# Kernel optimization log

Hardware: AMD Instinct MI355X
Metric: run time of the kernel (lower is better)

The kernel has to match this reference:

```python
import jax, jax.numpy as jnp
import numpy as np

N_HEAD = 12
N_EMBD = 768
HEAD_DIM = N_EMBD // N_HEAD
B, S = 4, 2048


def setup_inputs() -> dict:
    key = jax.random.key(0)
    k1, k2, k3, k4, k5 = jax.random.split(key, 5)
    x = jax.random.normal(k1, (B, S, N_EMBD), dtype=jnp.float32)
    # causal additive mask: 1.0 where attention is disallowed (strictly upper triangle)
    mask = (1.0 - jnp.tril(jnp.ones((S, S), dtype=jnp.float32)))[None, None, :, :]
    scale = 0.02
    W_attn = jax.random.normal(k2, (N_EMBD, 3 * N_EMBD), dtype=jnp.float32) * scale
    b_attn = jnp.zeros((3 * N_EMBD,), dtype=jnp.float32)
    W_proj = jax.random.normal(k3, (N_EMBD, N_EMBD), dtype=jnp.float32) * scale
    b_proj = jnp.zeros((N_EMBD,), dtype=jnp.float32)
    return {"x": x, "mask": mask, "W_attn": W_attn, "b_attn": b_attn,
            "W_proj": W_proj, "b_proj": b_proj}


def reference(x, mask, W_attn, b_attn, W_proj, b_proj):
    Bn, Sn, _ = x.shape
    qkv = x @ W_attn + b_attn                      # [B,S,3E]
    q, k, v = jnp.split(qkv, 3, axis=-1)           # each [B,S,E]

    def heads(t):
        return t.reshape(Bn, Sn, N_HEAD, HEAD_DIM).transpose(0, 2, 1, 3)  # [B,H,S,D]

    q, k, v = heads(q), heads(k), heads(v)
    attn = jnp.einsum('bhqd,bhkd->bhqk', q, k) / jnp.sqrt(jnp.float32(HEAD_DIM))
    attn = attn + mask * (-1e9)
    attn = jax.nn.softmax(attn, axis=-1)
    # dropout in inference mode = identity
    out = jnp.einsum('bhqk,bhkd->bhqd', attn, v)   # [B,H,S,D]
    out = out.transpose(0, 2, 1, 3).reshape(Bn, Sn, N_EMBD)
    return out @ W_proj + b_proj
```

## Files before the change

### kernel.cpp

```cpp
#include <hip/hip_runtime.h>
#include <stdint.h>

#define NHEAD 12
#define HDIM  64
#define EMB   768
#define N3    2304
#define SEQ   2048
#define BATCH 4
#define MROWS 8192

#define QSCALE 0.18033688011112042f

typedef __bf16 bf16_t;
typedef __bf16 bf16x8 __attribute__((ext_vector_type(8)));
typedef __bf16 bf16x4 __attribute__((ext_vector_type(4)));
typedef short  s16x4  __attribute__((ext_vector_type(4)));
typedef float  f32x4  __attribute__((ext_vector_type(4)));

__device__ __forceinline__ void gld_lds16(void* lds, const void* g) {
    __builtin_amdgcn_global_load_lds((const __attribute__((address_space(1))) void*)g,
                                     (__attribute__((address_space(3))) void*)lds,
                                     16, 0, 0);
}

__device__ __forceinline__ float fast_exp2(float x) {
    return __builtin_amdgcn_exp2f(x);
}

__device__ __forceinline__ f32x4 mfma16_bf16(bf16x4 a, bf16x4 b, f32x4 c) {
#if __has_builtin(__builtin_amdgcn_mfma_f32_16x16x16_bf16)
    return __builtin_amdgcn_mfma_f32_16x16x16_bf16(a, b, c, 0, 0, 0);
#else
    union U { bf16x4 h; s16x4 s; };
    U ua, ub; ua.h = a; ub.h = b;
    return __builtin_amdgcn_mfma_f32_16x16x16bf16_1k(ua.s, ub.s, c, 0, 0, 0);
#endif
}

__global__ __launch_bounds__(256) void cvt_x_k(const float* __restrict__ x,
                                               bf16_t* __restrict__ xb, int n8) {
    int idx    = blockIdx.x * blockDim.x + threadIdx.x;
    int stride = gridDim.x * blockDim.x;
    for (int i = idx; i < n8; i += stride) {
        float4 a = ((const float4*)x)[i * 2];
        float4 b = ((const float4*)x)[i * 2 + 1];
        bf16x8 v;
        v[0] = (bf16_t)a.x; v[1] = (bf16_t)a.y; v[2] = (bf16_t)a.z; v[3] = (bf16_t)a.w;
        v[4] = (bf16_t)b.x; v[5] = (bf16_t)b.y; v[6] = (bf16_t)b.z; v[7] = (bf16_t)b.w;
        ((bf16x8*)xb)[i] = v;
    }
}

__global__ __launch_bounds__(256) void transpose_cvt_k(
    const float* __restrict__ W, bf16_t* __restrict__ WT, int K, int N) {
    __shared__ float tile[32][33];
    const int n0 = blockIdx.x * 32, k0 = blockIdx.y * 32;
    const int tx = threadIdx.x & 31, ty = threadIdx.x >> 5;
#pragma unroll
    for (int i = 0; i < 32; i += 8)
        tile[ty + i][tx] = W[(size_t)(k0 + ty + i) * N + (n0 + tx)];
    __syncthreads();
#pragma unroll
    for (int i = 0; i < 32; i += 8)
        WT[(size_t)(n0 + ty + i) * K + (k0 + tx)] = (bf16_t)tile[tx][ty + i];
}

template<int MODE>
__global__ __launch_bounds__(256) void gemm_kernel(
    const bf16_t* __restrict__ Av,
    const bf16_t* __restrict__ BT,
    const float* __restrict__ bias,
    float* __restrict__ out,
    bf16_t* __restrict__ qbuf,
    bf16_t* __restrict__ kbuf,
    bf16_t* __restrict__ vbuf,
    int Ncols)
{
    const int K = 768;
    __shared__ alignas(16) bf16_t As[2][128 * 32];
    __shared__ alignas(16) bf16_t Bs[2][128 * 32];

    const int tid    = threadIdx.x;
    const int wave   = tid >> 6;
    const int lane   = tid & 63;
    const int lane15 = lane & 15;
    const int quad   = lane >> 4;

    const int mBase = blockIdx.y * 128;
    const int nBase = blockIdx.x * 128;
    const int wm = (wave >> 1) * 64;
    const int wn = (wave & 1) * 64;

    f32x4 acc[4][4];
#pragma unroll
    for (int i = 0; i < 4; i++)
#pragma unroll
        for (int j = 0; j < 4; j++) acc[i][j] = (f32x4){0.f, 0.f, 0.f, 0.f};

    const bf16_t* aSrc = Av + (size_t)mBase * K;
    const bf16_t* bSrc = BT + (size_t)nBase * K;

    const int srow = lane >> 2;
    const int sch  = lane & 3;

    auto issueA = [&](int k0, int buf) {
#pragma unroll
        for (int p = 0; p < 2; p++) {
            int r0  = p * 64 + wave * 16;
            int row = r0 + srow;
            int lch = sch ^ (row & 3);
            gld_lds16(&As[buf][r0 * 32], aSrc + (size_t)row * K + k0 + lch * 8);
        }
    };
    auto issueB = [&](int k0, int buf) {
#pragma unroll
        for (int p = 0; p < 2; p++) {
            int r0  = p * 64 + wave * 16;
            int row = r0 + srow;
            int lch = sch ^ (row & 3);
            gld_lds16(&Bs[buf][r0 * 32], bSrc + (size_t)row * K + k0 + lch * 8);
        }
    };

    issueA(0, 0);
    issueB(0, 0);

    for (int k0 = 0, it = 0; k0 < K; k0 += 32, it++) {
        const int buf = it & 1;
        __syncthreads();
        if (k0 + 32 < K) {
            issueB(k0 + 32, buf ^ 1);
            issueA(k0 + 32, buf ^ 1);
        }

        bf16x8 aF[4], bF[4];
#pragma unroll
        for (int t = 0; t < 4; t++) {
            int ra = wm + t * 16 + lane15;
            int rb = wn + t * 16 + lane15;
            aF[t] = *(const bf16x8*)&As[buf][ra * 32 + (quad ^ (ra & 3)) * 8];
            bF[t] = *(const bf16x8*)&Bs[buf][rb * 32 + (quad ^ (rb & 3)) * 8];
        }
#pragma unroll
        for (int i = 0; i < 4; i++)
#pragma unroll
            for (int j = 0; j < 4; j++)
                acc[i][j] = __builtin_amdgcn_mfma_f32_16x16x32_bf16(aF[i], bF[j], acc[i][j], 0, 0, 0);
    }

    const int region = (MODE == 1) ? (nBase / EMB) : 0;
#pragma unroll
    for (int i = 0; i < 4; i++) {
#pragma unroll
        for (int j = 0; j < 4; j++) {
            int gn = nBase + wn + j * 16 + lane15;
            float bv = bias[gn];
            if (MODE == 0) {
#pragma unroll
                for (int r = 0; r < 4; r++) {
                    int gm = mBase + wm + i * 16 + quad * 4 + r;
                    out[(size_t)gm * Ncols + gn] = acc[i][j][r] + bv;
                }
            } else if (region == 2) {
                int within = gn - 2 * EMB;
                int h = within >> 6, d = within & 63;
                int gm0 = mBase + wm + i * 16 + quad * 4;
                int b = gm0 >> 11, s = gm0 & 2047;
                int bh = b * NHEAD + h;
                bf16x4 v4;
#pragma unroll
                for (int r = 0; r < 4; r++) v4[r] = (bf16_t)(acc[i][j][r] + bv);
                *(bf16x4*)&vbuf[((size_t)bh * HDIM + d) * SEQ + s] = v4;
            } else {
                bf16_t* dst = (region == 0) ? qbuf : kbuf;
                const float scale = (region == 0) ? QSCALE : 1.0f;
                int within = gn - region * EMB;
                int h = within >> 6, d = within & 63;
#pragma unroll
                for (int r = 0; r < 4; r++) {
                    int gm = mBase + wm + i * 16 + quad * 4 + r;
                    int b = gm >> 11, s = gm & 2047;
                    int bh = b * NHEAD + h;
                    dst[((size_t)bh * SEQ + s) * HDIM + d] = (bf16_t)((acc[i][j][r] + bv) * scale);
                }
            }
        }
    }
}

__global__ __launch_bounds__(256) void attn_kernel(
    const bf16_t* __restrict__ qbuf,
    const bf16_t* __restrict__ kbuf,
    const bf16_t* __restrict__ vtbuf,
    bf16_t* __restrict__ obuf)
{
    __shared__ alignas(16) bf16_t Ks[2][64 * 64];
    __shared__ alignas(16) bf16_t Vs[2][64 * 64];
    __shared__ alignas(16) bf16_t Plds[4][16 * 72];

    const int tid    = threadIdx.x;
    const int wave   = tid >> 6;
    const int lane   = tid & 63;
    const int lane15 = lane & 15;
    const int quad   = lane >> 4;

    const int bh = blockIdx.x >> 4;
    const int j  = blockIdx.x & 15;

    const bf16_t* Qp = qbuf  + (size_t)bh * SEQ * HDIM;
    const bf16_t* Kp = kbuf  + (size_t)bh * SEQ * HDIM;
    const bf16_t* Vp = vtbuf + (size_t)bh * HDIM * SEQ;
    bf16_t* pl = &Plds[wave][0];
    const int b = bh / NHEAD, h = bh % NHEAD;

    const int srow8 = lane >> 3;
    const int sch8  = lane & 7;

    auto issueKV = [&](int kb, int buf) {
#pragma unroll
        for (int p = 0; p < 2; p++) {
            int r0  = p * 32 + wave * 8;
            int row = r0 + srow8;
            int lch = sch8 ^ (row & 7);
            gld_lds16(&Ks[buf][r0 * 64], Kp + (size_t)(kb + row) * HDIM + lch * 8);
            gld_lds16(&Vs[buf][r0 * 64], Vp + (size_t)row * SEQ + kb + lch * 8);
        }
    };

    for (int seg = 0; seg < 2; seg++) {
        const int qt = seg ? (31 - j) : j;
        const int q0 = qt * 64 + wave * 16;

        const bf16x8 qf0 = *(const bf16x8*)&Qp[(size_t)(q0 + lane15) * HDIM + quad * 8];
        const bf16x8 qf1 = *(const bf16x8*)&Qp[(size_t)(q0 + lane15) * HDIM + 32 + quad * 8];

        float lrow = 0.f;
        f32x4 oT[4];
#pragma unroll
        for (int t = 0; t < 4; t++) oT[t] = (f32x4){0.f, 0.f, 0.f, 0.f};

        const int nT = qt + 1;
        __syncthreads();
        issueKV(0, 0);

        for (int kt = 0; kt < nT; kt++) {
            const int buf = kt & 1;
            __syncthreads();
            if (kt + 1 < nT) issueKV((kt + 1) * 64, buf ^ 1);

            const int kb = kt * 64;

            f32x4 sT[4];
#pragma unroll
            for (int kg = 0; kg < 4; kg++) {
                sT[kg] = (f32x4){0.f, 0.f, 0.f, 0.f};
                int row = kg * 16 + lane15;
                bf16x8 kf0 = *(const bf16x8*)&Ks[buf][row * 64 + ((quad    ) ^ (row & 7)) * 8];
                bf16x8 kf1 = *(const bf16x8*)&Ks[buf][row * 64 + ((quad + 4) ^ (row & 7)) * 8];
                sT[kg] = __builtin_amdgcn_mfma_f32_16x16x32_bf16(kf0, qf0, sT[kg], 0, 0, 0);
                sT[kg] = __builtin_amdgcn_mfma_f32_16x16x32_bf16(kf1, qf1, sT[kg], 0, 0, 0);
            }

            if (kb + 64 > q0) {
                const int query = q0 + lane15;
#pragma unroll
                for (int kg = 0; kg < 4; kg++) {
                    int key0 = kb + kg * 16 + quad * 4;
#pragma unroll
                    for (int r = 0; r < 4; r++)
                        sT[kg][r] = (key0 + r <= query) ? sT[kg][r] : -1e30f;
                }
            }

            bf16x4 pf[4];
#pragma unroll
            for (int kg = 0; kg < 4; kg++) {
#pragma unroll
                for (int r = 0; r < 4; r++) sT[kg][r] = fast_exp2(sT[kg][r]);
                lrow += (sT[kg][0] + sT[kg][1]) + (sT[kg][2] + sT[kg][3]);
                bf16x4 v;
#pragma unroll
                for (int r = 0; r < 4; r++) v[r] = (bf16_t)sT[kg][r];
                pf[kg] = v;
            }

#pragma unroll
            for (int t = 0; t < 4; t++) {
                int vrow = t * 16 + lane15;
#pragma unroll
                for (int kg = 0; kg < 4; kg++) {
                    int c    = kg * 2 + (quad >> 1);
                    int phys = c ^ (vrow & 7);
                    bf16x4 vf = *(const bf16x4*)&Vs[buf][vrow * 64 + phys * 8 + (quad & 1) * 4];
                    oT[t] = mfma16_bf16(vf, pf[kg], oT[t]);
                }
            }
        }

        lrow += __shfl_xor(lrow, 16, 64);
        lrow += __shfl_xor(lrow, 32, 64);
        const float inv = 1.0f / lrow;

#pragma unroll
        for (int t = 0; t < 4; t++)
#pragma unroll
            for (int r = 0; r < 4; r++)
                pl[lane15 * 72 + t * 16 + quad * 4 + r] = (bf16_t)(oT[t][r] * inv);

        const int qrow = lane >> 2;
        const int ch   = lane & 3;
        bf16_t* orow = &obuf[((size_t)(b * SEQ + q0 + qrow)) * EMB + h * HDIM];
#pragma unroll
        for (int p = 0; p < 2; p++) {
            bf16x8 v = *(const bf16x8*)&pl[qrow * 72 + (ch + p * 4) * 8];
            *(bf16x8*)&orow[(ch + p * 4) * 8] = v;
        }
    }
}

extern "C" void kernel_launch(void* const* d_in, const int* in_sizes, int n_in,
                              void* d_out, int out_size, void* d_ws, size_t ws_size,
                              hipStream_t stream) {
    const float* x      = (const float*)d_in[0];
    const float* W_attn = (const float*)d_in[2];
    const float* b_attn = (const float*)d_in[3];
    const float* W_proj = (const float*)d_in[4];
    const float* b_proj = (const float*)d_in[5];
    float* out = (float*)d_out;

    bf16_t* ws  = (bf16_t*)d_ws;
    bf16_t* WaT = ws;
    bf16_t* WpT = WaT + (size_t)N3 * EMB;
    bf16_t* Qb  = WpT + (size_t)EMB * EMB;
    bf16_t* Kb  = Qb + (size_t)BATCH * NHEAD * SEQ * HDIM;
    bf16_t* Vt  = Kb + (size_t)BATCH * NHEAD * SEQ * HDIM;
    bf16_t* Ob  = Vt + (size_t)BATCH * NHEAD * SEQ * HDIM;
    bf16_t* xb  = Ob;

    transpose_cvt_k<<<dim3(N3 / 32, EMB / 32), 256, 0, stream>>>(W_attn, WaT, EMB, N3);
    transpose_cvt_k<<<dim3(EMB / 32, EMB / 32), 256, 0, stream>>>(W_proj, WpT, EMB, EMB);
    cvt_x_k<<<1536, 256, 0, stream>>>(x, xb, MROWS * EMB / 8);

    gemm_kernel<1><<<dim3(N3 / 128, MROWS / 128), 256, 0, stream>>>(
        xb, WaT, b_attn, nullptr, Qb, Kb, Vt, N3);

    attn_kernel<<<BATCH * NHEAD * 16, 256, 0, stream>>>(Qb, Kb, Vt, Ob);

    gemm_kernel<0><<<dim3(EMB / 128, MROWS / 128), 256, 0, stream>>>(
        Ob, WpT, b_proj, out, nullptr, nullptr, nullptr, EMB);
}
```

Measured before the change: 246.1 us.

## Add dedicated 256x256-tile pipelined QKV GEMM kernel with 8 waves

Replaces the generic 128x128 GEMM used for the QKV projection with a dedicated kernel. It uses 256x256 output tiles, 512 threads, a K-step of 64 with double-buffered direct-to-LDS loads, and phased prefetch interleaved with MFMA work under s_setprio. It also remaps block indices so that consecutive blocks share data in cache. The goal is more data reuse per loaded tile and better overlap of memory loads with compute. In exchange, register and LDS pressure rises (256KB LDS per block is not possible; uses 2*2*128*64*2*2=128KB), and there are only 288 blocks, so occupancy and tail effects may suffer.

```diff
diff --git a/kernel.cpp b/kernel.cpp
--- a/kernel.cpp
+++ b/kernel.cpp
@@ -65,15 +65,176 @@
         WT[(size_t)(n0 + ty + i) * K + (k0 + tx)] = (bf16_t)tile[tx][ty + i];
 }
 
+__global__ __launch_bounds__(512, 2) void qkv_kernel(
+    const bf16_t* __restrict__ Av,
+    const bf16_t* __restrict__ BT,
+    const float*  __restrict__ bias,
+    bf16_t* __restrict__ qbuf,
+    bf16_t* __restrict__ kbuf,
+    bf16_t* __restrict__ vbuf)
+{
+    __shared__ alignas(16) bf16_t As[2][2][128 * 64];
+    __shared__ alignas(16) bf16_t Bs[2][2][128 * 64];
+
+    const int tid    = threadIdx.x;
+    const int wave   = tid >> 6;
+    const int lane   = tid & 63;
+    const int lane15 = lane & 15;
+    const int quad   = lane >> 4;
+    const int wr     = wave >> 2;
+    const int wc     = wave & 3;
+
+    const int bid  = blockIdx.x;
+    const int swz  = (bid & 7) * 36 + (bid >> 3);
+    const int mBase = (swz / 9) * 256;
+    const int nBase = (swz % 9) * 256;
+
+    const int rr = tid >> 3;
+    const int ch = (tid & 7) ^ (rr & 7);
+    const bf16_t* aBase = Av + (size_t)mBase * 768;
+    const bf16_t* bBase = BT + (size_t)nBase * 768;
+
+    auto stageA = [&](int kt, int h) {
+        const int buf = kt & 1;
+#pragma unroll
+        for (int p = 0; p < 2; p++) {
+            const bf16_t* src = aBase + (size_t)(h * 128 + p * 64 + rr) * 768 + kt * 64 + ch * 8;
+            gld_lds16(&As[buf][h][p * 4096 + wave * 512], src);
+        }
+    };
+    auto stageB = [&](int kt, int h) {
+        const int buf = kt & 1;
+#pragma unroll
+        for (int p = 0; p < 2; p++) {
+            const bf16_t* src = bBase + (size_t)(h * 128 + p * 64 + rr) * 768 + kt * 64 + ch * 8;
+            gld_lds16(&Bs[buf][h][p * 4096 + wave * 512], src);
+        }
+    };
+
+    f32x4 acc[8][4];
+#pragma unroll
+    for (int m = 0; m < 8; m++)
+#pragma unroll
+        for (int n = 0; n < 4; n++) acc[m][n] = (f32x4){0.f, 0.f, 0.f, 0.f};
+
+    bf16x8 bF[4][2];
+
+    stageA(0, 0); stageA(0, 1); stageB(0, 0); stageB(0, 1); stageB(1, 0);
+
+    for (int t = 0; t < 12; ++t) {
+        const int buf = t & 1;
+        const bf16_t* Ah = &As[buf][wr][0];
+        const bf16_t* Bh = &Bs[buf][wc >> 1][0];
+
+        if (t < 11) {
+            stageB(t + 1, 1);
+            asm volatile("s_waitcnt vmcnt(4)" ::: "memory");
+        } else {
+            asm volatile("s_waitcnt vmcnt(0)" ::: "memory");
+        }
+        __builtin_amdgcn_sched_barrier(0);
+        __builtin_amdgcn_s_barrier();
+
+#pragma unroll
+        for (int n = 0; n < 4; ++n) {
+            const int rb = (wc & 1) * 64 + n * 16 + lane15;
+#pragma unroll
+            for (int kk = 0; kk < 2; ++kk)
+                bF[n][kk] = *(const bf16x8*)&Bh[rb * 64 + (((kk * 4 + quad) ^ (rb & 7)) * 8)];
+        }
+        {
+            bf16x8 aF[2][2];
+#pragma unroll
+            for (int mm = 0; mm < 2; ++mm) {
+                const int r = mm * 16 + lane15;
+#pragma unroll
+                for (int kk = 0; kk < 2; ++kk)
+                    aF[mm][kk] = *(const bf16x8*)&Ah[r * 64 + (((kk * 4 + quad) ^ (r & 7)) * 8)];
+            }
+            __builtin_amdgcn_s_setprio(1);
+#pragma unroll
+            for (int mm = 0; mm < 2; ++mm)
+#pragma unroll
+                for (int n = 0; n < 4; ++n)
+#pragma unroll
+                    for (int kk = 0; kk < 2; ++kk)
+                        acc[mm][n] = __builtin_amdgcn_mfma_f32_16x16x32_bf16(aF[mm][kk], bF[n][kk], acc[mm][n], 0, 0, 0);
+            __builtin_amdgcn_s_setprio(0);
+            __builtin_amdgcn_s_barrier();
+        }
+
+#define QKV_PHASE(Q, STAGE_STMT)                                                          \
+        {                                                                                 \
+            STAGE_STMT;                                                                   \
+            bf16x8 aF[2][2];                                                              \
+            _Pragma("unroll")                                                             \
+            for (int mm = 0; mm < 2; ++mm) {                                              \
+                const int r = (Q) * 32 + mm * 16 + lane15;                                \
+                _Pragma("unroll")                                                         \
+                for (int kk = 0; kk < 2; ++kk)                                            \
+                    aF[mm][kk] = *(const bf16x8*)&Ah[r * 64 + (((kk * 4 + quad) ^ (r & 7)) * 8)]; \
+            }                                                                             \
+            __builtin_amdgcn_s_barrier();                                                 \
+            __builtin_amdgcn_s_setprio(1);                                                \
+            _Pragma("unroll")                                                             \
+            for (int mm = 0; mm < 2; ++mm)                                                \
+                _Pragma("unroll")                                                         \
+                for (int n = 0; n < 4; ++n)                                               \
+                    _Pragma("unroll")                                                     \
+                    for (int kk = 0; kk < 2; ++kk)                                        \
+                        acc[(Q) * 2 + mm][n] = __builtin_amdgcn_mfma_f32_16x16x32_bf16(   \
+                            aF[mm][kk], bF[n][kk], acc[(Q) * 2 + mm][n], 0, 0, 0);        \
+            __builtin_amdgcn_s_setprio(0);                                                \
+            __builtin_amdgcn_s_barrier();                                                 \
+        }
+
+        QKV_PHASE(1, if (t < 11) stageA(t + 1, 0))
+        QKV_PHASE(2, if (t < 11) stageA(t + 1, 1))
+        QKV_PHASE(3, if (t < 10) stageB(t + 2, 0))
+#undef QKV_PHASE
+    }
+
+    const int region = nBase / EMB;
+#pragma unroll
+    for (int n = 0; n < 4; ++n) {
+        const int gn = nBase + wc * 64 + n * 16 + lane15;
+        const float bv = bias[gn];
+        const int within = gn - region * EMB;
+        const int h = within >> 6, d = within & 63;
+        if (region == 2) {
+#pragma unroll
+            for (int m = 0; m < 8; ++m) {
+                const int gm0 = mBase + wr * 128 + m * 16 + quad * 4;
+                const int b = gm0 >> 11, s = gm0 & 2047;
+                const int bh = b * NHEAD + h;
+                bf16x4 v4;
+#pragma unroll
+                for (int r = 0; r < 4; ++r) v4[r] = (bf16_t)(acc[m][n][r] + bv);
+                *(bf16x4*)&vbuf[((size_t)bh * HDIM + d) * SEQ + s] = v4;
+            }
+        } else {
+            bf16_t* dst = (region == 0) ? qbuf : kbuf;
+            const float scale = (region == 0) ? QSCALE : 1.0f;
+#pragma unroll
+            for (int m = 0; m < 8; ++m) {
+#pragma unroll
+                for (int r = 0; r < 4; ++r) {
+                    const int gm = mBase + wr * 128 + m * 16 + quad * 4 + r;
+                    const int b = gm >> 11, s = gm & 2047;
+                    const int bh = b * NHEAD + h;
+                    dst[((size_t)bh * SEQ + s) * HDIM + d] = (bf16_t)((acc[m][n][r] + bv) * scale);
+                }
+            }
+        }
+    }
+}
+
 template<int MODE>
 __global__ __launch_bounds__(256) void gemm_kernel(
     const bf16_t* __restrict__ Av,
     const bf16_t* __restrict__ BT,
     const float* __restrict__ bias,
     float* __restrict__ out,
-    bf16_t* __restrict__ qbuf,
-    bf16_t* __restrict__ kbuf,
-    bf16_t* __restrict__ vbuf,
     int Ncols)
 {
     const int K = 768;
@@ -148,41 +309,16 @@
                 acc[i][j] = __builtin_amdgcn_mfma_f32_16x16x32_bf16(aF[i], bF[j], acc[i][j], 0, 0, 0);
     }
 
-    const int region = (MODE == 1) ? (nBase / EMB) : 0;
 #pragma unroll
     for (int i = 0; i < 4; i++) {
 #pragma unroll
         for (int j = 0; j < 4; j++) {
             int gn = nBase + wn + j * 16 + lane15;
             float bv = bias[gn];
-            if (MODE == 0) {
-#pragma unroll
-                for (int r = 0; r < 4; r++) {
-                    int gm = mBase + wm + i * 16 + quad * 4 + r;
-                    out[(size_t)gm * Ncols + gn] = acc[i][j][r] + bv;
-                }
-            } else if (region == 2) {
-                int within = gn - 2 * EMB;
-                int h = within >> 6, d = within & 63;
-                int gm0 = mBase + wm + i * 16 + quad * 4;
-                int b = gm0 >> 11, s = gm0 & 2047;
-                int bh = b * NHEAD + h;
-                bf16x4 v4;
-#pragma unroll
-                for (int r = 0; r < 4; r++) v4[r] = (bf16_t)(acc[i][j][r] + bv);
-                *(bf16x4*)&vbuf[((size_t)bh * HDIM + d) * SEQ + s] = v4;
-            } else {
-                bf16_t* dst = (region == 0) ? qbuf : kbuf;
-                const float scale = (region == 0) ? QSCALE : 1.0f;
-                int within = gn - region * EMB;
-                int h = within >> 6, d = within & 63;
-#pragma unroll
-                for (int r = 0; r < 4; r++) {
-                    int gm = mBase + wm + i * 16 + quad * 4 + r;
-                    int b = gm >> 11, s = gm & 2047;
-                    int bh = b * NHEAD + h;
-                    dst[((size_t)bh * SEQ + s) * HDIM + d] = (bf16_t)((acc[i][j][r] + bv) * scale);
-                }
+#pragma unroll
+            for (int r = 0; r < 4; r++) {
+                int gm = mBase + wm + i * 16 + quad * 4 + r;
+                out[(size_t)gm * Ncols + gn] = acc[i][j][r] + bv;
             }
         }
     }
@@ -341,11 +477,10 @@
     transpose_cvt_k<<<dim3(EMB / 32, EMB / 32), 256, 0, stream>>>(W_proj, WpT, EMB, EMB);
     cvt_x_k<<<1536, 256, 0, stream>>>(x, xb, MROWS * EMB / 8);
 
-    gemm_kernel<1><<<dim3(N3 / 128, MROWS / 128), 256, 0, stream>>>(
-        xb, WaT, b_attn, nullptr, Qb, Kb, Vt, N3);
+    qkv_kernel<<<288, 512, 0, stream>>>(xb, WaT, b_attn, Qb, Kb, Vt);
 
     attn_kernel<<<BATCH * NHEAD * 16, 256, 0, stream>>>(Qb, Kb, Vt, Ob);
 
     gemm_kernel<0><<<dim3(EMB / 128, MROWS / 128), 256, 0, stream>>>(
-        Ob, WpT, b_proj, out, nullptr, nullptr, nullptr, EMB);
-}
+        Ob, WpT, b_proj, out, EMB);
+}
```

New measurement: 269.4 us. 1.09x slower.
